# Performance work log

Measured on AMD Instinct MI355X. Metric: run time of the kernel, lower is better.

## Reference

```python
import jax, jax.numpy as jnp
import numpy as np

N = 100000
E = 1600000
F_IN = 100
H = 64
C = 18
K = 2  # num_stacks
T = 2  # num_layers


def setup_inputs() -> dict:
    key = jax.random.key(0)
    ks = jax.random.split(key, 12)
    def glorot(k, shape):
        fan = shape[-2] + shape[-1]
        s = jnp.sqrt(6.0 / fan)
        return jax.random.uniform(k, shape, jnp.float32, -s, s)
    return {
        "x": jax.random.normal(ks[0], (N, F_IN), jnp.float32),
        "edge_index": jax.random.randint(ks[1], (2, E), 0, N, jnp.int64),
        "init_w1": glorot(ks[2], (K, F_IN, H)),
        "w1": glorot(ks[3], (K, H, H)),
        "root_w1": glorot(ks[4], (K, F_IN, H)),
        "b1": jnp.zeros((K, 1, H), jnp.float32),
        "init_w2": glorot(ks[5], (K, H, C)),
        "w2": glorot(ks[6], (K, C, C)),
        "root_w2": glorot(ks[7], (K, H, C)),
        "b2": jnp.zeros((K, 1, C), jnp.float32),
    }


def _gcn_norm(src, tgt):
    # symmetric normalization, no self loops (PyG ARMAConv default)
    deg = jax.ops.segment_sum(jnp.ones((E,), jnp.float32), tgt, num_segments=N)
    dis = jnp.where(deg > 0, jax.lax.rsqrt(jnp.maximum(deg, 1.0)), 0.0)
    return dis[src] * dis[tgt]  # [E]


def _arma_conv(x, src, tgt, norm, init_w, w, root_w, b):
    # x: [N, Fin]; returns [N, Fout]
    root = jnp.einsum('nf,kfh->knh', x, root_w)  # [K, N, Fout] (shared across layers)
    out = None
    for t in range(T):
        if t == 0:
            h = jnp.einsum('nf,kfh->knh', x, init_w)
        else:
            h = jnp.einsum('knh,khg->kng', out, w)
        # gather-scale-scatter propagation per stack
        msgs = h[:, src, :] * norm[None, :, None]  # [K, E, Fout]
        agg = jax.vmap(lambda m: jax.ops.segment_sum(m, tgt, num_segments=N))(msgs)
        out = jax.nn.relu(agg + root + b)
    return out.mean(axis=0)  # mean over stacks


def reference(x, edge_index, init_w1, w1, root_w1, b1, init_w2, w2, root_w2, b2):
    src, tgt = edge_index[0], edge_index[1]
    norm = _gcn_norm(src, tgt)
    h = jax.nn.relu(_arma_conv(x, src, tgt, norm, init_w1, w1, root_w1, b1))
    out = _arma_conv(h, src, tgt, norm, init_w2, w2, root_w2, b2)
    return jax.nn.log_softmax(out, axis=-1)
```

## Files before the change

### kernel.cpp

```cpp
#include <hip/hip_runtime.h>
#include <hip/hip_bf16.h>
#include <math.h>

#define N_NODES 100000
#define N_EDGES 1600000
#define F_IN 100
#define H 64
#define C 18
#define BSHIFT 8
#define BSIZE 256
#define NBUCKETS ((N_NODES + BSIZE - 1) >> BSHIFT)
#define NBLK 256
#define CHUNK (N_EDGES / NBLK)

typedef __attribute__((ext_vector_type(8))) short v8s;
typedef __attribute__((ext_vector_type(4))) float v4f;
typedef __attribute__((ext_vector_type(2))) float v2f;


__device__ __forceinline__ unsigned bf16_rne(float f) {
    unsigned u = __float_as_uint(f);
    return (u + 0x7FFFu + ((u >> 16) & 1u)) >> 16;
}
__device__ __forceinline__ unsigned pack_bf2(float a, float b) {
    return bf16_rne(a) | (bf16_rne(b) << 16);
}
__device__ __forceinline__ float2 unpack_bf2(unsigned u) {
    return make_float2(__uint_as_float(u << 16), __uint_as_float(u & 0xFFFF0000u));
}
__device__ __forceinline__ ushort pack_fp8x2(float a, float b) {
    int r = __builtin_amdgcn_cvt_pk_fp8_f32(a, b, 0, false);
    return (ushort)(r & 0xFFFF);
}
__device__ __forceinline__ float2 unpack_fp8x2(ushort u) {
    v2f r = __builtin_amdgcn_cvt_pk_f32_fp8((int)u, false);
    return make_float2(r[0], r[1]);
}


__global__ void scan1_kernel(const int* __restrict__ cnt, int* __restrict__ excl,
                             int* __restrict__ bsum, int n) {
    __shared__ int tmp[256];
    int t = threadIdx.x;
    int i = blockIdx.x * 256 + t;
    int v = (i < n) ? cnt[i] : 0;
    tmp[t] = v;
    __syncthreads();
    for (int off = 1; off < 256; off <<= 1) {
        int xv = (t >= off) ? tmp[t - off] : 0;
        __syncthreads();
        tmp[t] += xv;
        __syncthreads();
    }
    if (i < n) excl[i] = tmp[t] - v;
    if (t == 255) bsum[blockIdx.x] = tmp[255];
}

__global__ void __launch_bounds__(512) scan2p_prep_kernel(
        int* __restrict__ bsum, int nb,
        const float* __restrict__ iw1, const float* __restrict__ rw1,
        const float* __restrict__ w1,  const float* __restrict__ iw2,
        const float* __restrict__ rw2, const float* __restrict__ w2,
        ushort* __restrict__ W1T, ushort* __restrict__ WmT,
        ushort* __restrict__ W2T, ushort* __restrict__ W3T) {
    int t = threadIdx.x;
    if (blockIdx.x == 0) {
        __shared__ int s[512];
        int v = (t < nb) ? bsum[t] : 0;
        s[t] = v;
        __syncthreads();
        for (int off = 1; off < 512; off <<= 1) {
            int xv = (t >= off) ? s[t - off] : 0;
            __syncthreads();
            s[t] += xv;
            __syncthreads();
        }
        if (t < nb) bsum[t] = s[t] - v;
        return;
    }
    int gid = (blockIdx.x - 1) * 512 + t;
    if (gid < 32768) {
        int idx = gid;
        int m = idx >> 13, nn = (idx >> 7) & 63, kk = idx & 127;
        int stk = m & 1, isWr = m >> 1;
        float v = 0.f;
        if (kk < F_IN) v = (isWr ? rw1 : iw1)[((size_t)stk * F_IN + kk) * 64 + nn];
        W1T[idx] = (ushort)bf16_rne(v);
    } else if (gid < 32768 + 8192) {
        int idx = gid - 32768;
        int stk = idx >> 12, g = (idx >> 6) & 63, f = idx & 63;
        WmT[idx] = (ushort)bf16_rne(w1[((size_t)stk * 64 + f) * 64 + g]);
    } else if (gid < 32768 + 8192 + 8192) {
        int idx = gid - 32768 - 8192;
        int m = idx >> 11, col = (idx >> 6) & 31, k = idx & 63;
        int stk = m & 1, isWr = m >> 1;
        float v = 0.f;
        if (col < C) v = (isWr ? rw2 : iw2)[((size_t)stk * H + k) * C + col];
        W2T[idx] = (ushort)bf16_rne(v);
    } else if (gid < 32768 + 8192 + 8192 + 2048) {
        int idx = gid - 32768 - 8192 - 8192;
        int stk = idx >> 10, col = (idx >> 5) & 31, k = idx & 31;
        float v = 0.f;
        if (col < C && k < C) v = w2[((size_t)stk * C + k) * C + col];
        W3T[idx] = (ushort)bf16_rne(v);
    }
}


__global__ void __launch_bounds__(256) histA_kernel(const int* __restrict__ tgt,
                                                    int* __restrict__ hist) {
    __shared__ int h[NBUCKETS];
    int blk = blockIdx.x, t = threadIdx.x;
    for (int i = t; i < NBUCKETS; i += 256) h[i] = 0;
    __syncthreads();
    int e0 = blk * CHUNK, e1 = e0 + CHUNK;
    for (int e = e0 + t; e < e1; e += 256) atomicAdd(&h[tgt[e] >> BSHIFT], 1);
    __syncthreads();
    for (int i = t; i < NBUCKETS; i += 256) hist[i * NBLK + blk] = h[i];
}

__global__ void __launch_bounds__(256) scatterC_kernel(
        const int* __restrict__ src, const int* __restrict__ tgt,
        const int* __restrict__ histx, const int* __restrict__ bsum,
        unsigned* __restrict__ tmp) {
    __shared__ int cur[NBUCKETS];
    int blk = blockIdx.x, t = threadIdx.x;
    for (int i = t; i < NBUCKETS; i += 256) {
        int gi = i * NBLK + blk;
        cur[i] = histx[gi] + bsum[gi >> 8];
    }
    __syncthreads();
    int e0 = blk * CHUNK, e1 = e0 + CHUNK;
    for (int e = e0 + t; e < e1; e += 256) {
        int s = src[e], tg = tgt[e];
        int b = tg >> BSHIFT;
        int pos = atomicAdd(&cur[b], 1);
        tmp[pos] = (unsigned)s | ((unsigned)(tg & (BSIZE - 1)) << 17);
    }
}

__global__ void __launch_bounds__(256) bucketD2_kernel(
        const unsigned* __restrict__ tmp, const int* __restrict__ histx,
        const int* __restrict__ bsum,
        int* __restrict__ rp, float* __restrict__ dinv, int* __restrict__ ssrc) {
    __shared__ int cnt_l[BSIZE];
    __shared__ int scan_l[BSIZE];
    int b = blockIdx.x;
    int t = threadIdx.x;
    int gi_lo = b * NBLK;
    int e_lo = histx[gi_lo] + bsum[gi_lo >> 8];
    int e_hi = N_EDGES;
    if (b + 1 < NBUCKETS) {
        int gi_hi = (b + 1) * NBLK;
        e_hi = histx[gi_hi] + bsum[gi_hi >> 8];
    }
    int n_lo = b << BSHIFT;
    int n_hi = min(n_lo + BSIZE, N_NODES);
    int nn = n_hi - n_lo;
    cnt_l[t] = 0;
    __syncthreads();
    for (int e = e_lo + t; e < e_hi; e += 256)
        atomicAdd(&cnt_l[(int)(tmp[e] >> 17)], 1);
    __syncthreads();
    int v = cnt_l[t];
    scan_l[t] = v;
    __syncthreads();
    for (int off = 1; off < 256; off <<= 1) {
        int xv = (t >= off) ? scan_l[t - off] : 0;
        __syncthreads();
        scan_l[t] += xv;
        __syncthreads();
    }
    int my_start = e_lo + scan_l[t] - v;
    if (t < nn) {
        rp[n_lo + t] = my_start;
        dinv[n_lo + t] = (v > 0) ? rsqrtf((float)v) : 0.f;
    }
    if (b == NBUCKETS - 1 && t == 0) rp[N_NODES] = N_EDGES;
    __syncthreads();
    cnt_l[t] = my_start;
    __syncthreads();
    for (int e = e_lo + t; e < e_hi; e += 256) {
        unsigned p = tmp[e];
        int s = (int)(p & 0x1FFFFu);
        int tl = (int)(p >> 17);
        int pos = atomicAdd(&cnt_l[tl], 1);
        ssrc[pos] = s;
    }
}


__global__ void __launch_bounds__(256) dense1_mfma(
        const float* __restrict__ x, const ushort* __restrict__ W1T,
        const float* __restrict__ dinv,
        ushort* __restrict__ g, unsigned* __restrict__ root) {
    __shared__ char xs[32 * 256];
    int tid = threadIdx.x;
    int b0 = blockIdx.x * 32;
    for (int i = tid; i < 32 * 25; i += 256) {
        int row = i / 25, f4 = i - row * 25;
        int grow = b0 + row;
        float4 v = make_float4(0.f, 0.f, 0.f, 0.f);
        if (grow < N_NODES) v = *(const float4*)(x + (size_t)grow * F_IN + f4 * 4);
        unsigned p0 = pack_bf2(v.x, v.y);
        unsigned p1 = pack_bf2(v.z, v.w);
        int pr = f4 * 2;
        int gr = (pr >> 2) ^ (row & 7);
        char* base = xs + row * 256 + (gr << 4) + (pr & 3) * 4;
        *(unsigned*)base = p0;
        *(unsigned*)(base + 4) = p1;
    }
    for (int i = tid; i < 32 * 14; i += 256) {
        int row = i / 14, pr = 50 + (i - row * 14);
        int gr = (pr >> 2) ^ (row & 7);
        *(unsigned*)(xs + row * 256 + (gr << 4) + (pr & 3) * 4) = 0;
    }
    __syncthreads();
    int lane = tid & 63;
    int w = __builtin_amdgcn_readfirstlane(tid >> 6);
    int q = lane >> 4, cl = lane & 15;
    int isWr = w >> 1;
    int colbase = (w & 1) * 32;
    v8s bfr[2][2][4];
    #pragma unroll
    for (int stk = 0; stk < 2; ++stk)
        #pragma unroll
        for (int nt = 0; nt < 2; ++nt)
            #pragma unroll
            for (int ks = 0; ks < 4; ++ks) {
                const ushort* p = W1T + ((size_t)(isWr * 2 + stk) * 64 + colbase + nt * 16 + cl) * 128
                                  + ks * 32 + q * 8;
                bfr[stk][nt][ks] = *(const v8s*)p;
            }
    #pragma unroll
    for (int mt = 0; mt < 2; ++mt) {
        v8s afr[4];
        #pragma unroll
        for (int ks = 0; ks < 4; ++ks) {
            int row = mt * 16 + cl;
            int gr = (ks * 4 + q) ^ (row & 7);
            afr[ks] = *(const v8s*)(xs + row * 256 + (gr << 4));
        }
        v4f acc[2][2];
        #pragma unroll
        for (int stk = 0; stk < 2; ++stk)
            #pragma unroll
            for (int nt = 0; nt < 2; ++nt) {
                v4f a = {0.f, 0.f, 0.f, 0.f};
                #pragma unroll
                for (int ks = 0; ks < 4; ++ks)
                    a = __builtin_amdgcn_mfma_f32_16x16x32_bf16(afr[ks], bfr[stk][nt][ks], a, 0, 0, 0);
                acc[stk][nt] = a;
            }
        #pragma unroll
        for (int nt = 0; nt < 2; ++nt)
            #pragma unroll
            for (int reg = 0; reg < 4; ++reg) {
                int node = b0 + mt * 16 + q * 4 + reg;
                if (node < N_NODES) {
                    int col = colbase + nt * 16 + cl;
                    if (isWr == 0) {
                        float dv = dinv[node];
                        g[(size_t)node * 64 + col] = pack_fp8x2(dv * acc[0][nt][reg], dv * acc[1][nt][reg]);
                    } else {
                        root[(size_t)node * 64 + col] = pack_bf2(acc[0][nt][reg], acc[1][nt][reg]);
                    }
                }
            }
    }
}

__global__ void __launch_bounds__(256) dense_mid_mfma(
        const ushort* __restrict__ hk0, const ushort* __restrict__ hk1,
        const ushort* __restrict__ WmT, const float* __restrict__ dinv,
        ushort* __restrict__ g2) {
    __shared__ char hs[2 * 64 * 128];
    int tid = threadIdx.x;
    int b0 = blockIdx.x * 64;
    for (int i = tid; i < 1024; i += 256) {
        int stk = i >> 9, rem = i & 511, row = rem >> 3, gr = rem & 7;
        int grow = b0 + row;
        uint4 v = make_uint4(0, 0, 0, 0);
        const ushort* srcp = stk ? hk1 : hk0;
        if (grow < N_NODES) v = *(const uint4*)(srcp + (size_t)grow * 64 + gr * 8);
        *(uint4*)(hs + stk * 8192 + row * 128 + ((gr ^ (row & 7)) << 4)) = v;
    }
    __syncthreads();
    int lane = tid & 63;
    int w = __builtin_amdgcn_readfirstlane(tid >> 6);
    int q = lane >> 4, cl = lane & 15;
    v8s bfr[2][2];
    #pragma unroll
    for (int stk = 0; stk < 2; ++stk)
        #pragma unroll
        for (int ks = 0; ks < 2; ++ks)
            bfr[stk][ks] = *(const v8s*)(WmT + ((size_t)stk * 64 + w * 16 + cl) * 64 + ks * 32 + q * 8);
    #pragma unroll
    for (int mt = 0; mt < 4; ++mt) {
        v4f acc[2];
        #pragma unroll
        for (int stk = 0; stk < 2; ++stk) {
            v4f a = {0.f, 0.f, 0.f, 0.f};
            #pragma unroll
            for (int ks = 0; ks < 2; ++ks) {
                int row = mt * 16 + cl;
                int gr = (ks * 4 + q) ^ (row & 7);
                v8s af = *(const v8s*)(hs + stk * 8192 + row * 128 + (gr << 4));
                a = __builtin_amdgcn_mfma_f32_16x16x32_bf16(af, bfr[stk][ks], a, 0, 0, 0);
            }
            acc[stk] = a;
        }
        #pragma unroll
        for (int reg = 0; reg < 4; ++reg) {
            int node = b0 + mt * 16 + q * 4 + reg;
            if (node < N_NODES) {
                float dv = dinv[node];
                g2[(size_t)node * 64 + w * 16 + cl] = pack_fp8x2(dv * acc[0][reg], dv * acc[1][reg]);
            }
        }
    }
}

__global__ void __launch_bounds__(256) dense_y2_mfma(
        const ushort* __restrict__ yb, const ushort* __restrict__ W2T,
        const float* __restrict__ dinv,
        ushort* __restrict__ h2, unsigned* __restrict__ root2) {
    __shared__ char ys[64 * 128];
    int tid = threadIdx.x;
    int b0 = blockIdx.x * 64;
    for (int i = tid; i < 512; i += 256) {
        int row = i >> 3, gr = i & 7;
        int grow = b0 + row;
        uint4 v = make_uint4(0, 0, 0, 0);
        if (grow < N_NODES) v = *(const uint4*)(yb + (size_t)grow * 64 + gr * 8);
        *(uint4*)(ys + row * 128 + ((gr ^ (row & 7)) << 4)) = v;
    }
    __syncthreads();
    int lane = tid & 63;
    int w = __builtin_amdgcn_readfirstlane(tid >> 6);
    int q = lane >> 4, cl = lane & 15;
    int isWr = w >> 1;
    int mbase = (w & 1) * 2;
    v8s bfr[2][2][2];
    #pragma unroll
    for (int stk = 0; stk < 2; ++stk)
        #pragma unroll
        for (int nt = 0; nt < 2; ++nt)
            #pragma unroll
            for (int ks = 0; ks < 2; ++ks)
                bfr[stk][nt][ks] = *(const v8s*)(W2T + ((size_t)(isWr * 2 + stk) * 32 + nt * 16 + cl) * 64
                                                 + ks * 32 + q * 8);
    #pragma unroll
    for (int mi = 0; mi < 2; ++mi) {
        int mt = mbase + mi;
        v8s afr[2];
        #pragma unroll
        for (int ks = 0; ks < 2; ++ks) {
            int row = mt * 16 + cl;
            int gr = (ks * 4 + q) ^ (row & 7);
            afr[ks] = *(const v8s*)(ys + row * 128 + (gr << 4));
        }
        v4f acc[2][2];
        #pragma unroll
        for (int stk = 0; stk < 2; ++stk)
            #pragma unroll
            for (int nt = 0; nt < 2; ++nt) {
                v4f a = {0.f, 0.f, 0.f, 0.f};
                #pragma unroll
                for (int ks = 0; ks < 2; ++ks)
                    a = __builtin_amdgcn_mfma_f32_16x16x32_bf16(afr[ks], bfr[stk][nt][ks], a, 0, 0, 0);
                acc[stk][nt] = a;
            }
        #pragma unroll
        for (int nt = 0; nt < 2; ++nt)
            #pragma unroll
            for (int reg = 0; reg < 4; ++reg) {
                int node = b0 + mt * 16 + q * 4 + reg;
                int col = nt * 16 + cl;
                if (node < N_NODES && col < C) {
                    if (isWr == 0) {
                        float dv = dinv[node];
                        h2[(size_t)node * C + col] = pack_fp8x2(dv * acc[0][nt][reg], dv * acc[1][nt][reg]);
                    } else {
                        root2[(size_t)node * C + col] = pack_bf2(acc[0][nt][reg], acc[1][nt][reg]);
                    }
                }
            }
    }
}

__global__ void __launch_bounds__(256) dense_last_mfma(
        const ushort* __restrict__ ok0, const ushort* __restrict__ ok1,
        const ushort* __restrict__ W3T, const float* __restrict__ dinv,
        ushort* __restrict__ h3) {
    __shared__ char hs[2 * 64 * 64];
    int tid = threadIdx.x;
    int b0 = blockIdx.x * 64;
    for (int i = tid; i < 2048; i += 256) ((unsigned*)hs)[i] = 0;
    __syncthreads();
    for (int i = tid; i < 4096; i += 256) {
        int stk = i >> 11, row = (i >> 5) & 63, col = i & 31;
        int node = b0 + row;
        if (col < C && node < N_NODES) {
            ushort v = (stk ? ok1 : ok0)[(size_t)node * C + col];
            int gr = (col >> 3) ^ (row & 3);
            *(ushort*)(hs + stk * 4096 + row * 64 + (gr << 4) + (col & 7) * 2) = v;
        }
    }
    __syncthreads();
    int lane = tid & 63;
    int w = __builtin_amdgcn_readfirstlane(tid >> 6);
    int q = lane >> 4, cl = lane & 15;
    v8s bfr[2][2];
    #pragma unroll
    for (int stk = 0; stk < 2; ++stk)
        #pragma unroll
        for (int nt = 0; nt < 2; ++nt)
            bfr[stk][nt] = *(const v8s*)(W3T + ((size_t)stk * 32 + nt * 16 + cl) * 32 + q * 8);
    int row = w * 16 + cl;
    int gr = q ^ (row & 3);
    v8s af0 = *(const v8s*)(hs + row * 64 + (gr << 4));
    v8s af1 = *(const v8s*)(hs + 4096 + row * 64 + (gr << 4));
    v4f acc[2][2];
    #pragma unroll
    for (int nt = 0; nt < 2; ++nt) {
        acc[0][nt] = __builtin_amdgcn_mfma_f32_16x16x32_bf16(af0, bfr[0][nt], (v4f){0.f,0.f,0.f,0.f}, 0, 0, 0);
        acc[1][nt] = __builtin_amdgcn_mfma_f32_16x16x32_bf16(af1, bfr[1][nt], (v4f){0.f,0.f,0.f,0.f}, 0, 0, 0);
    }
    #pragma unroll
    for (int nt = 0; nt < 2; ++nt)
        #pragma unroll
        for (int reg = 0; reg < 4; ++reg) {
            int node = b0 + w * 16 + q * 4 + reg;
            int col = nt * 16 + cl;
            if (node < N_NODES && col < C) {
                float dv = dinv[node];
                h3[(size_t)node * C + col] = pack_fp8x2(dv * acc[0][nt][reg], dv * acc[1][nt][reg]);
            }
        }
}


template <int FINAL>
__global__ void __launch_bounds__(256) prop64_kernel(
        const ushort* __restrict__ g, const unsigned* __restrict__ root,
        const float* __restrict__ b, const float* __restrict__ dinv,
        const int* __restrict__ rp, const int* __restrict__ ssrc,
        ushort* __restrict__ ok0, ushort* __restrict__ ok1, ushort* __restrict__ yb) {
    int lane = threadIdx.x & 63;
    int wid = __builtin_amdgcn_readfirstlane((int)((blockIdx.x * 256 + threadIdx.x) >> 6));
    if (wid >= N_NODES) return;
    int e0 = rp[wid], e1 = rp[wid + 1];
    bool hi = lane >= 32;
    int c32 = lane & 31;
    const unsigned* g32 = (const unsigned*)g;
    uint2 rtu = *(const uint2*)(root + (size_t)wid * H + 2 * c32);
    float dv = dinv[wid];
    float bA0 = b[2 * c32], bB0 = b[2 * c32 + 1];
    float bA1 = b[H + 2 * c32], bB1 = b[H + 2 * c32 + 1];
    float aA0 = 0.f, aA1 = 0.f, aB0 = 0.f, aB1 = 0.f;
    int e = e0;
    for (; e + 16 <= e1; e += 16) {
        unsigned u[8];
        #pragma unroll
        for (int j = 0; j < 8; ++j) {
            int s0 = ssrc[e + 2 * j];
            int s1 = ssrc[e + 2 * j + 1];
            int srow = hi ? s1 : s0;
            u[j] = g32[(size_t)srow * 32 + c32];
        }
        #pragma unroll
        for (int j = 0; j < 8; ++j) {
            float2 vA = unpack_fp8x2((ushort)(u[j] & 0xFFFFu));
            float2 vB = unpack_fp8x2((ushort)(u[j] >> 16));
            aA0 += vA.x; aA1 += vA.y; aB0 += vB.x; aB1 += vB.y;
        }
    }
    for (; e + 2 <= e1; e += 2) {
        int s0 = ssrc[e];
        int s1 = ssrc[e + 1];
        int srow = hi ? s1 : s0;
        unsigned u = g32[(size_t)srow * 32 + c32];
        float2 vA = unpack_fp8x2((ushort)(u & 0xFFFFu));
        float2 vB = unpack_fp8x2((ushort)(u >> 16));
        aA0 += vA.x; aA1 += vA.y; aB0 += vB.x; aB1 += vB.y;
    }
    if (e < e1) {
        int s0 = ssrc[e];
        unsigned u = g32[(size_t)s0 * 32 + c32];
        if (!hi) {
            float2 vA = unpack_fp8x2((ushort)(u & 0xFFFFu));
            float2 vB = unpack_fp8x2((ushort)(u >> 16));
            aA0 += vA.x; aA1 += vA.y; aB0 += vB.x; aB1 += vB.y;
        }
    }
    aA0 += __shfl_xor(aA0, 32, 64);
    aA1 += __shfl_xor(aA1, 32, 64);
    aB0 += __shfl_xor(aB0, 32, 64);
    aB1 += __shfl_xor(aB1, 32, 64);
    if (lane < 32) {
        float2 rtA = unpack_bf2(rtu.x);
        float2 rtB = unpack_bf2(rtu.y);
        float oA0 = fmaxf(fmaf(dv, aA0, rtA.x + bA0), 0.f);
        float oA1 = fmaxf(fmaf(dv, aA1, rtA.y + bA1), 0.f);
        float oB0 = fmaxf(fmaf(dv, aB0, rtB.x + bB0), 0.f);
        float oB1 = fmaxf(fmaf(dv, aB1, rtB.y + bB1), 0.f);
        size_t base = (size_t)wid * H + 2 * c32;
        if (FINAL) {
            *(unsigned*)(yb + base) = pack_bf2(0.5f * (oA0 + oA1), 0.5f * (oB0 + oB1));
        } else {
            *(unsigned*)(ok0 + base) = pack_bf2(oA0, oB0);
            *(unsigned*)(ok1 + base) = pack_bf2(oA1, oB1);
        }
    }
}

template <int FINAL>
__global__ void __launch_bounds__(256) prop18_kernel(
        const ushort* __restrict__ g, const unsigned* __restrict__ root,
        const float* __restrict__ b, const float* __restrict__ dinv,
        const int* __restrict__ rp, const int* __restrict__ ssrc,
        ushort* __restrict__ ok0, ushort* __restrict__ ok1, float* __restrict__ outp) {
    int lane = threadIdx.x & 63;
    int wid = __builtin_amdgcn_readfirstlane((int)((blockIdx.x * 256 + threadIdx.x) >> 6));
    if (wid >= N_NODES) return;
    int e0 = rp[wid], e1 = rp[wid + 1];
    bool hi = lane >= 32;
    int c32 = lane & 31;
    bool actG = c32 < C;
    int c = actG ? c32 : 0;
    unsigned rtu = root[(size_t)wid * C + c];
    float dv = dinv[wid];
    float bl0 = b[c], bl1 = b[C + c];
    float a0 = 0.f, a1 = 0.f;
    int e = e0;
    for (; e + 16 <= e1; e += 16) {
        ushort u[8];
        #pragma unroll
        for (int j = 0; j < 8; ++j) {
            int s0 = ssrc[e + 2 * j];
            int s1 = ssrc[e + 2 * j + 1];
            int srow = hi ? s1 : s0;
            u[j] = g[(size_t)srow * C + c];
        }
        if (actG) {
            #pragma unroll
            for (int j = 0; j < 8; ++j) { float2 v = unpack_fp8x2(u[j]); a0 += v.x; a1 += v.y; }
        }
    }
    for (; e + 2 <= e1; e += 2) {
        int s0 = ssrc[e];
        int s1 = ssrc[e + 1];
        int srow = hi ? s1 : s0;
        float2 v = unpack_fp8x2(g[(size_t)srow * C + c]);
        if (actG) { a0 += v.x; a1 += v.y; }
    }
    if (e < e1) {
        int s0 = ssrc[e];
        float2 v = unpack_fp8x2(g[(size_t)s0 * C + c]);
        if (actG && !hi) { a0 += v.x; a1 += v.y; }
    }
    a0 += __shfl_xor(a0, 32, 64);
    a1 += __shfl_xor(a1, 32, 64);
    bool actO = lane < C;
    if (!FINAL) {
        if (actO) {
            float2 rt = unpack_bf2(rtu);
            float o0 = fmaxf(fmaf(dv, a0, rt.x + bl0), 0.f);
            float o1 = fmaxf(fmaf(dv, a1, rt.y + bl1), 0.f);
            ok0[(size_t)wid * C + c] = (ushort)bf16_rne(o0);
            ok1[(size_t)wid * C + c] = (ushort)bf16_rne(o1);
        }
    } else {
        float m = -INFINITY;
        if (actO) {
            float2 rt = unpack_bf2(rtu);
            float o0 = fmaxf(fmaf(dv, a0, rt.x + bl0), 0.f);
            float o1 = fmaxf(fmaf(dv, a1, rt.y + bl1), 0.f);
            m = 0.5f * (o0 + o1);
        }
        float mx = m;
        #pragma unroll
        for (int off = 16; off >= 1; off >>= 1) mx = fmaxf(mx, __shfl_xor(mx, off, 64));
        float ex = actO ? __expf(m - mx) : 0.f;
        float sum = ex;
        #pragma unroll
        for (int off = 16; off >= 1; off >>= 1) sum += __shfl_xor(sum, off, 64);
        if (actO) outp[(size_t)wid * C + c] = m - mx - logf(sum);
    }
}


extern "C" void kernel_launch(void* const* d_in, const int* in_sizes, int n_in,
                              void* d_out, int out_size, void* d_ws, size_t ws_size,
                              hipStream_t stream) {
    const float* x        = (const float*)d_in[0];
    const int*   ei       = (const int*)d_in[1];
    const float* init_w1  = (const float*)d_in[2];
    const float* w1       = (const float*)d_in[3];
    const float* root_w1  = (const float*)d_in[4];
    const float* b1       = (const float*)d_in[5];
    const float* init_w2  = (const float*)d_in[6];
    const float* w2       = (const float*)d_in[7];
    const float* root_w2  = (const float*)d_in[8];
    const float* b2       = (const float*)d_in[9];
    const int* src = ei;
    const int* tgt = ei + N_EDGES;
    float* out = (float*)d_out;

    char* w = (char*)d_ws;
    size_t off = 0;
    auto alloc = [&](size_t bytes) -> char* {
        char* p = w + off;
        off += (bytes + 255) & ~(size_t)255;
        return p;
    };
    int*      rp    = (int*)alloc((size_t)(N_NODES + 1) * 4);
    float*    dinv  = (float*)alloc((size_t)N_NODES * 4);
    int*      bsum  = (int*)alloc(512 * 4);
    int*      hist  = (int*)alloc((size_t)NBUCKETS * NBLK * 4);
    int*      histx = (int*)alloc((size_t)NBUCKETS * NBLK * 4);
    unsigned* tmp   = (unsigned*)alloc((size_t)N_EDGES * 4);
    int*      ssrc  = (int*)alloc((size_t)N_EDGES * 4);
    ushort*   W1T   = (ushort*)alloc((size_t)4 * 64 * 128 * 2);
    ushort*   WmT   = (ushort*)alloc((size_t)2 * 64 * 64 * 2);
    ushort*   W2T   = (ushort*)alloc((size_t)4 * 32 * 64 * 2);
    ushort*   W3T   = (ushort*)alloc((size_t)2 * 32 * 32 * 2);
    ushort*   g1    = (ushort*)alloc((size_t)N_NODES * H * 2);
    unsigned* root1 = (unsigned*)alloc((size_t)N_NODES * H * 4);
    ushort*   hk0   = (ushort*)alloc((size_t)N_NODES * H * 2);
    ushort*   hk1   = (ushort*)alloc((size_t)N_NODES * H * 2);
    ushort*   g2    = (ushort*)alloc((size_t)N_NODES * H * 2);
    ushort*   yb    = (ushort*)alloc((size_t)N_NODES * H * 2);
    ushort*   h2u   = (ushort*)alloc((size_t)N_NODES * C * 2);
    unsigned* root2u= (unsigned*)alloc((size_t)N_NODES * C * 4);
    ushort*   h3u   = (ushort*)alloc((size_t)N_NODES * C * 2);
    ushort*   p18k0 = (ushort*)g1;
    ushort*   p18k1 = (ushort*)g1 + (size_t)N_NODES * C;

    int nbH = (NBUCKETS * NBLK + 255) / 256;

    histA_kernel<<<NBLK, 256, 0, stream>>>(tgt, hist);
    scan1_kernel<<<nbH, 256, 0, stream>>>(hist, histx, bsum, NBUCKETS * NBLK);
    scan2p_prep_kernel<<<101, 512, 0, stream>>>(bsum, nbH,
                                                init_w1, root_w1, w1, init_w2, root_w2, w2,
                                                W1T, WmT, W2T, W3T);
    scatterC_kernel<<<NBLK, 256, 0, stream>>>(src, tgt, histx, bsum, tmp);
    bucketD2_kernel<<<NBUCKETS, 256, 0, stream>>>(tmp, histx, bsum, rp, dinv, ssrc);

    int g1blocks = (N_NODES + 31) / 32;
    int gblocks  = (N_NODES + 63) / 64;
    int pgrid    = (N_NODES + 3) / 4;

    dense1_mfma<<<g1blocks, 256, 0, stream>>>(x, W1T, dinv, g1, root1);
    prop64_kernel<0><<<pgrid, 256, 0, stream>>>(g1, root1, b1, dinv, rp, ssrc, hk0, hk1, nullptr);
    dense_mid_mfma<<<gblocks, 256, 0, stream>>>(hk0, hk1, WmT, dinv, g2);
    prop64_kernel<1><<<pgrid, 256, 0, stream>>>(g2, root1, b1, dinv, rp, ssrc, nullptr, nullptr, yb);

    dense_y2_mfma<<<gblocks, 256, 0, stream>>>(yb, W2T, dinv, h2u, root2u);
    prop18_kernel<0><<<pgrid, 256, 0, stream>>>(h2u, root2u, b2, dinv, rp, ssrc, p18k0, p18k1, nullptr);
    dense_last_mfma<<<gblocks, 256, 0, stream>>>(p18k0, p18k1, W3T, dinv, h3u);
    prop18_kernel<1><<<pgrid, 256, 0, stream>>>(h3u, root2u, b2, dinv, rp, ssrc, nullptr, nullptr, out);
}
```

Measured before the change: 309.6 us.

## Load x directly into MFMA fragments per wave, dropping LDS staging in dense1

Restructures the first dense kernel so each wave handles 16 nodes on its own and computes both the init and root products across all 64 columns. x is read from global memory straight into bf16 A-fragments, so the LDS buffer, its swizzled writes and the block barrier are gone. Weight fragments are now loaded inside the MFMA loop rather than held in registers, which increases weight traffic from L1/L2. The global x reads per lane are strided across rows and less coalesced than the previous staged loads.

```diff
diff --git a/kernel.cpp b/kernel.cpp
--- a/kernel.cpp
+++ b/kernel.cpp
@@ -194,77 +194,63 @@
         const float* __restrict__ x, const ushort* __restrict__ W1T,
         const float* __restrict__ dinv,
         ushort* __restrict__ g, unsigned* __restrict__ root) {
-    __shared__ char xs[32 * 256];
     int tid = threadIdx.x;
-    int b0 = blockIdx.x * 32;
-    for (int i = tid; i < 32 * 25; i += 256) {
-        int row = i / 25, f4 = i - row * 25;
-        int grow = b0 + row;
-        float4 v = make_float4(0.f, 0.f, 0.f, 0.f);
-        if (grow < N_NODES) v = *(const float4*)(x + (size_t)grow * F_IN + f4 * 4);
-        unsigned p0 = pack_bf2(v.x, v.y);
-        unsigned p1 = pack_bf2(v.z, v.w);
-        int pr = f4 * 2;
-        int gr = (pr >> 2) ^ (row & 7);
-        char* base = xs + row * 256 + (gr << 4) + (pr & 3) * 4;
-        *(unsigned*)base = p0;
-        *(unsigned*)(base + 4) = p1;
-    }
-    for (int i = tid; i < 32 * 14; i += 256) {
-        int row = i / 14, pr = 50 + (i - row * 14);
-        int gr = (pr >> 2) ^ (row & 7);
-        *(unsigned*)(xs + row * 256 + (gr << 4) + (pr & 3) * 4) = 0;
-    }
-    __syncthreads();
     int lane = tid & 63;
-    int w = __builtin_amdgcn_readfirstlane(tid >> 6);
+    int wv = blockIdx.x * 4 + (tid >> 6);
+    if (wv >= N_NODES / 16) return;
+    int b0 = wv * 16;
     int q = lane >> 4, cl = lane & 15;
-    int isWr = w >> 1;
-    int colbase = (w & 1) * 32;
-    v8s bfr[2][2][4];
-    #pragma unroll
-    for (int stk = 0; stk < 2; ++stk)
-        #pragma unroll
-        for (int nt = 0; nt < 2; ++nt)
-            #pragma unroll
-            for (int ks = 0; ks < 4; ++ks) {
-                const ushort* p = W1T + ((size_t)(isWr * 2 + stk) * 64 + colbase + nt * 16 + cl) * 128
-                                  + ks * 32 + q * 8;
-                bfr[stk][nt][ks] = *(const v8s*)p;
-            }
-    #pragma unroll
-    for (int mt = 0; mt < 2; ++mt) {
-        v8s afr[4];
-        #pragma unroll
-        for (int ks = 0; ks < 4; ++ks) {
-            int row = mt * 16 + cl;
-            int gr = (ks * 4 + q) ^ (row & 7);
-            afr[ks] = *(const v8s*)(xs + row * 256 + (gr << 4));
-        }
-        v4f acc[2][2];
+    int row = b0 + cl;
+    const float* xr = x + (size_t)row * F_IN;
+    v8s afr[4];
+    #pragma unroll
+    for (int ks = 0; ks < 3; ++ks) {
+        float4 va = *(const float4*)(xr + ks * 32 + q * 8);
+        float4 vb = *(const float4*)(xr + ks * 32 + q * 8 + 4);
+        unsigned p0 = pack_bf2(va.x, va.y), p1 = pack_bf2(va.z, va.w);
+        unsigned p2 = pack_bf2(vb.x, vb.y), p3 = pack_bf2(vb.z, vb.w);
+        unsigned* ap = (unsigned*)&afr[ks];
+        ap[0] = p0; ap[1] = p1; ap[2] = p2; ap[3] = p3;
+    }
+    {
+        unsigned* ap = (unsigned*)&afr[3];
+        if (q == 0) {
+            float4 va = *(const float4*)(xr + 96);
+            ap[0] = pack_bf2(va.x, va.y); ap[1] = pack_bf2(va.z, va.w);
+        } else { ap[0] = 0; ap[1] = 0; }
+        ap[2] = 0; ap[3] = 0;
+    }
+    float dvr[4];
+    #pragma unroll
+    for (int reg = 0; reg < 4; ++reg) dvr[reg] = dinv[b0 + q * 4 + reg];
+    #pragma unroll
+    for (int mat = 0; mat < 2; ++mat) {
+        v4f acc[2][4];
         #pragma unroll
         for (int stk = 0; stk < 2; ++stk)
             #pragma unroll
-            for (int nt = 0; nt < 2; ++nt) {
-                v4f a = {0.f, 0.f, 0.f, 0.f};
+            for (int nt = 0; nt < 4; ++nt) acc[stk][nt] = (v4f){0.f, 0.f, 0.f, 0.f};
+        #pragma unroll
+        for (int ks = 0; ks < 4; ++ks)
+            #pragma unroll
+            for (int stk = 0; stk < 2; ++stk)
                 #pragma unroll
-                for (int ks = 0; ks < 4; ++ks)
-                    a = __builtin_amdgcn_mfma_f32_16x16x32_bf16(afr[ks], bfr[stk][nt][ks], a, 0, 0, 0);
-                acc[stk][nt] = a;
-            }
-        #pragma unroll
-        for (int nt = 0; nt < 2; ++nt)
+                for (int nt = 0; nt < 4; ++nt) {
+                    v8s bf = *(const v8s*)(W1T + ((size_t)(mat * 2 + stk) * 64 + nt * 16 + cl) * 128
+                                           + ks * 32 + q * 8);
+                    acc[stk][nt] = __builtin_amdgcn_mfma_f32_16x16x32_bf16(afr[ks], bf, acc[stk][nt], 0, 0, 0);
+                }
+        #pragma unroll
+        for (int nt = 0; nt < 4; ++nt)
             #pragma unroll
             for (int reg = 0; reg < 4; ++reg) {
-                int node = b0 + mt * 16 + q * 4 + reg;
-                if (node < N_NODES) {
-                    int col = colbase + nt * 16 + cl;
-                    if (isWr == 0) {
-                        float dv = dinv[node];
-                        g[(size_t)node * 64 + col] = pack_fp8x2(dv * acc[0][nt][reg], dv * acc[1][nt][reg]);
-                    } else {
-                        root[(size_t)node * 64 + col] = pack_bf2(acc[0][nt][reg], acc[1][nt][reg]);
-                    }
+                int node = b0 + q * 4 + reg;
+                int col = nt * 16 + cl;
+                if (mat == 0) {
+                    g[(size_t)node * 64 + col] = pack_fp8x2(dvr[reg] * acc[0][nt][reg],
+                                                            dvr[reg] * acc[1][nt][reg]);
+                } else {
+                    root[(size_t)node * 64 + col] = pack_bf2(acc[0][nt][reg], acc[1][nt][reg]);
                 }
             }
     }
@@ -648,11 +634,11 @@
     scatterC_kernel<<<NBLK, 256, 0, stream>>>(src, tgt, histx, bsum, tmp);
     bucketD2_kernel<<<NBUCKETS, 256, 0, stream>>>(tmp, histx, bsum, rp, dinv, ssrc);
 
-    int g1blocks = (N_NODES + 31) / 32;
+    int d1blocks = (N_NODES / 16 + 3) / 4;
     int gblocks  = (N_NODES + 63) / 64;
     int pgrid    = (N_NODES + 3) / 4;
 
-    dense1_mfma<<<g1blocks, 256, 0, stream>>>(x, W1T, dinv, g1, root1);
+    dense1_mfma<<<d1blocks, 256, 0, stream>>>(x, W1T, dinv, g1, root1);
     prop64_kernel<0><<<pgrid, 256, 0, stream>>>(g1, root1, b1, dinv, rp, ssrc, hk0, hk1, nullptr);
     dense_mid_mfma<<<gblocks, 256, 0, stream>>>(hk0, hk1, WmT, dinv, g2);
     prop64_kernel<1><<<pgrid, 256, 0, stream>>>(g2, root1, b1, dinv, rp, ssrc, nullptr, nullptr, yb);
```

After: 327.6 us. 5.8% more time.
